# Kernel optimization log

Hardware: AMD Instinct MI355X
Metric: run time of the kernel (lower is better)

The kernel has to match this reference:

```python
import jax, jax.numpy as jnp
import numpy as np

EPS = 1e-3  # keras LayerNormalization default epsilon


def layer_norm(x, gamma, beta):
    mu = jnp.mean(x, axis=-1, keepdims=True)
    var = jnp.var(x, axis=-1, keepdims=True)
    return (x - mu) * jax.lax.rsqrt(var + EPS) * gamma + beta


def setup_inputs() -> dict:
    key = jax.random.key(0)
    ks = jax.random.split(key, 16)
    B, S, D = 8, 2048, 1024          # batch, seq, input_size
    P = 2 * D                        # up-projection dim (proj_factor=2)
    H = 1024                         # hidden = head_size(64) * num_heads(16)
    s = 0.02
    inp = {
        "x": jax.random.normal(ks[0], (B, S, D), jnp.float32),
        "ln1_g": jnp.ones((D,), jnp.float32),
        "ln1_b": jnp.zeros((D,), jnp.float32),
        "W_up": jax.random.normal(ks[1], (D, P), jnp.float32) * s,
        "b_up": jnp.zeros((P,), jnp.float32),
        "W_adj": jax.random.normal(ks[2], (P, H), jnp.float32) * s,
        "b_adj": jnp.zeros((H,), jnp.float32),
        "W_q": jax.random.normal(ks[3], (H, H), jnp.float32) * s,
        "b_q": jnp.zeros((H,), jnp.float32),
        "W_k": jax.random.normal(ks[4], (H, H), jnp.float32) * s,
        "b_k": jnp.zeros((H,), jnp.float32),
        "W_v": jax.random.normal(ks[5], (H, H), jnp.float32) * s,
        "b_v": jnp.zeros((H,), jnp.float32),
        "W_i": jax.random.normal(ks[6], (H, H), jnp.float32) * s,
        "b_i": jnp.zeros((H,), jnp.float32),
        "W_f": jax.random.normal(ks[7], (H, H), jnp.float32) * s,
        "b_f": jnp.zeros((H,), jnp.float32),
        "W_o": jax.random.normal(ks[8], (H, H), jnp.float32) * s,
        "b_o": jnp.zeros((H,), jnp.float32),
        "ln2_g": jnp.ones((H,), jnp.float32),
        "ln2_b": jnpos if False else jnp.zeros((H,), jnp.float32),
        "W_down": jax.random.normal(ks[9], (H, D), jnp.float32) * s,
        "b_down": jnp.zeros((D,), jnp.float32),
    }
    return inp


def reference(x, ln1_g, ln1_b, W_up, b_up, W_adj, b_adj,
              W_q, b_q, W_k, b_k, W_v, b_v,
              W_i, b_i, W_f, b_f, W_o, b_o,
              ln2_g, ln2_b, W_down, b_down):
    head_size = 64
    x_norm = layer_norm(x, ln1_g, ln1_b)
    x_up = x_norm @ W_up + b_up                      # [B,S,2D]
    x_adj = x_up @ W_adj + b_adj                     # [B,S,H]
    # BlockDiagonal layers: each block is a Dense over the FULL input,
    # concatenated -> equivalent to one [H,H] matmul with concatenated weights.
    q = x_adj @ W_q + b_q
    k = (x_adj @ W_k + b_k) / (head_size ** 0.5)
    v = x_adj @ W_v + b_v
    i_t = x_adj @ W_i + b_i
    f_t = x_adj @ W_f + b_f
    o = jax.nn.sigmoid(x_adj @ W_o + b_o)
    m_t = jnp.maximum(f_t, i_t)
    f = jnp.exp(f_t - m_t)                           # (i = exp(i_t - m_t) unused downstream)
    c_t = f * v * k
    h_t = o * (c_t * q) / jnp.maximum(jnp.abs(k * q), 1.0)
    out = layer_norm(h_t, ln2_g, ln2_b) * jax.nn.sigmoid(x_adj)
    out = out @ W_down + b_down
    return out + x
```

## Files before the change

kernel.cpp:

```cpp
#include <hip/hip_runtime.h>


typedef unsigned short u16;
typedef __attribute__((ext_vector_type(4))) unsigned short u16x4;
typedef __attribute__((ext_vector_type(8))) unsigned short u16x8;
typedef __attribute__((ext_vector_type(8))) __bf16 bf16x8;
typedef __attribute__((ext_vector_type(4))) float f32x4;

__device__ __forceinline__ float bf2f(u16 u) {
    union { unsigned int i; float f; } c; c.i = ((unsigned int)u) << 16; return c.f;
}
__device__ __forceinline__ u16 f2bf(float f) {
    union { float f; unsigned int i; } c; c.f = f;
    unsigned int lsb = (c.i >> 16) & 1u;
    c.i += 0x7fffu + lsb;
    return (u16)(c.i >> 16);
}
__device__ __forceinline__ float sigmoidf(float z) {
    return 1.0f / (1.0f + __expf(-z));
}

#define GLDS16(gp, lp)                                                        \
    __builtin_amdgcn_global_load_lds(                                         \
        (__attribute__((address_space(1))) void*)(void*)(gp),                 \
        (__attribute__((address_space(3))) void*)(lp), 16, 0, 0)

#define BM 128
#define BN 128
#define BK 32

template <int MODE>
__global__ __launch_bounds__(256) void gemm_bt(
    const u16* __restrict__ A, const u16* __restrict__ Bt,
    const float* __restrict__ bias, const float* __restrict__ resid,
    void* __restrict__ out, int M, int N, int K, float scale)
{
    __shared__ __align__(16) u16 As[2 * BM * BK];
    __shared__ __align__(16) u16 Bs[2 * BN * BK];

    const int tid  = threadIdx.x;
    const int lane = tid & 63;
    const int wave = tid >> 6;
    const int l15  = lane & 15;
    const int quad = lane >> 4;

    const long bm = (long)blockIdx.y * BM;
    const long bn = (long)blockIdx.x * BN;
    const int  wm = (wave >> 1) * 64;
    const int  wn = (wave & 1) * 64;

    f32x4 acc[4][4] = {};

    const int  r0 = tid >> 2;
    const int  ck = (((tid & 3) ^ ((tid >> 3) & 3)) * 8);
    const u16* ga0 = A  + (bm + r0) * (long)K + ck;
    const u16* gb0 = Bt + (bn + r0) * (long)K + ck;
    const int  ldst = wave * 512;

    auto stage = [&](int t_, int b_) {
        const long kof = (long)t_ * BK;
        u16* dA = &As[b_ * (BM * BK) + ldst];
        u16* dB = &Bs[b_ * (BN * BK) + ldst];
        GLDS16(ga0 + kof, dA);
        GLDS16(ga0 + kof + 64 * (long)K, dA + 2048);
        GLDS16(gb0 + kof, dB);
        GLDS16(gb0 + kof + 64 * (long)K, dB + 2048);
    };

    const int q8s = (quad ^ ((l15 >> 1) & 3)) * 8;
    const int nk  = K / BK;

    stage(0, 0);
    stage(1, 1);

    for (int t = 0; t < nk; ++t) {
        const int cur = t & 1;
        if (t + 1 < nk) asm volatile("s_waitcnt vmcnt(4)" ::: "memory");
        else            asm volatile("s_waitcnt vmcnt(0)" ::: "memory");
        __builtin_amdgcn_s_barrier();

        bf16x8 af[4], bfr[4];
#pragma unroll
        for (int t4 = 0; t4 < 4; ++t4) {
            af[t4]  = *(const bf16x8*)&As[cur * (BM * BK) + (wm + t4 * 16 + l15) * BK + q8s];
            bfr[t4] = *(const bf16x8*)&Bs[cur * (BN * BK) + (wn + t4 * 16 + l15) * BK + q8s];
        }
        asm volatile("s_waitcnt lgkmcnt(0)" ::: "memory");
        __builtin_amdgcn_s_barrier();
        if (t + 2 < nk) stage(t + 2, cur);

        __builtin_amdgcn_s_setprio(1);
#pragma unroll
        for (int mt = 0; mt < 4; ++mt)
#pragma unroll
            for (int nt = 0; nt < 4; ++nt)
                acc[mt][nt] = __builtin_amdgcn_mfma_f32_16x16x32_bf16(
                    af[mt], bfr[nt], acc[mt][nt], 0, 0, 0);
        __builtin_amdgcn_s_setprio(0);
    }

#pragma unroll
    for (int nt = 0; nt < 4; ++nt) {
        const long n  = bn + wn + nt * 16 + l15;
        const float bv = (MODE == 2) ? 0.0f : bias[n];
#pragma unroll
        for (int mt = 0; mt < 4; ++mt) {
            const long m0 = bm + wm + mt * 16 + quad * 4;
#pragma unroll
            for (int r = 0; r < 4; ++r) {
                const long idx = (m0 + r) * N + n;
                const float val = (acc[mt][nt][r] + bv) * scale;
                if (MODE == 1) ((float*)out)[idx] = val + resid[idx];
                else           ((u16*)out)[idx] = f2bf(val);
            }
        }
    }
}

__global__ __launch_bounds__(256) void gemm_gates(
    const u16* __restrict__ A, const u16* __restrict__ Wcat,
    const float* __restrict__ bq_, const float* __restrict__ bk_,
    const float* __restrict__ bv_, const float* __restrict__ bi_,
    const float* __restrict__ bf_, const float* __restrict__ bo_,
    u16* __restrict__ ht, int M, int N, int K)
{
    __shared__ __align__(16) u16 As[2 * 128 * 64];
    __shared__ __align__(16) u16 Bs[2 * 6 * 32 * 64];

    const int tid  = threadIdx.x;
    const int lane = tid & 63;
    const int wave = tid >> 6;
    const int l15  = lane & 15;
    const int quad = lane >> 4;

    const long bm = (long)blockIdx.y * 128;
    const long bn = (long)blockIdx.x * 32;

    f32x4 acc[6][4] = {};

    const int  rr = lane >> 3;
    const int  ck = (((lane & 7) ^ rr) * 8);

    const u16* gaj[4];
    int lAo[4];
#pragma unroll
    for (int j = 0; j < 4; ++j) {
        const int c = wave * 4 + j;
        gaj[j] = A + (bm + c * 8 + rr) * (long)K + ck;
        lAo[j] = c * 512;
    }
    const u16* gbj[6];
    int lBo[6];
#pragma unroll
    for (int j = 0; j < 6; ++j) {
        const int c = wave * 6 + j;
        const int g = c >> 2;
        const int r = (c & 3) * 8 + rr;
        gbj[j] = Wcat + ((long)g * 1024 + bn + r) * (long)K + ck;
        lBo[j] = c * 512;
    }

    auto stage = [&](int t_, int b_) {
        const long kof = (long)t_ * 64;
#pragma unroll
        for (int j = 0; j < 4; ++j)
            GLDS16(gaj[j] + kof, &As[b_ * 8192 + lAo[j]]);
#pragma unroll
        for (int j = 0; j < 6; ++j)
            GLDS16(gbj[j] + kof, &Bs[b_ * 12288 + lBo[j]]);
    };

    const int mh = (wave >> 1) * 64;
    const int nb = (wave & 1) * 16;
    const int l7 = l15 & 7;
    const int nk = K >> 6;

    stage(0, 0);
    stage(1, 1);

    for (int t = 0; t < nk; ++t) {
        const int cur = t & 1;
        if (t + 1 < nk) asm volatile("s_waitcnt vmcnt(10)" ::: "memory");
        else            asm volatile("s_waitcnt vmcnt(0)"  ::: "memory");
        __builtin_amdgcn_s_barrier();

        const int ab = cur * 8192;
        const int bb = cur * 12288;

        {
            const int so = (quad ^ l7) * 8;
            bf16x8 af[4];
#pragma unroll
            for (int t4 = 0; t4 < 4; ++t4)
                af[t4] = *(const bf16x8*)&As[ab + (mh + t4 * 16 + l15) * 64 + so];
            __builtin_amdgcn_s_setprio(1);
#pragma unroll
            for (int g = 0; g < 6; ++g) {
                const bf16x8 bfrag =
                    *(const bf16x8*)&Bs[bb + (g * 32 + nb + l15) * 64 + so];
#pragma unroll
                for (int t4 = 0; t4 < 4; ++t4)
                    acc[g][t4] = __builtin_amdgcn_mfma_f32_16x16x32_bf16(
                        af[t4], bfrag, acc[g][t4], 0, 0, 0);
            }
            __builtin_amdgcn_s_setprio(0);
        }
        bf16x8 af1[4], bf1[6];
        {
            const int so = ((4 + quad) ^ l7) * 8;
#pragma unroll
            for (int t4 = 0; t4 < 4; ++t4)
                af1[t4] = *(const bf16x8*)&As[ab + (mh + t4 * 16 + l15) * 64 + so];
#pragma unroll
            for (int g = 0; g < 6; ++g)
                bf1[g] = *(const bf16x8*)&Bs[bb + (g * 32 + nb + l15) * 64 + so];
        }
        asm volatile("s_waitcnt lgkmcnt(0)" ::: "memory");
        __builtin_amdgcn_s_barrier();
        if (t + 2 < nk) stage(t + 2, cur);

        __builtin_amdgcn_s_setprio(1);
#pragma unroll
        for (int g = 0; g < 6; ++g)
#pragma unroll
            for (int t4 = 0; t4 < 4; ++t4)
                acc[g][t4] = __builtin_amdgcn_mfma_f32_16x16x32_bf16(
                    af1[t4], bf1[g], acc[g][t4], 0, 0, 0);
        __builtin_amdgcn_s_setprio(0);
    }

    const long n = bn + nb + l15;
    const float bqn = bq_[n], bkn = bk_[n], bvn = bv_[n];
    const float bin = bi_[n], bfn = bf_[n], bon = bo_[n];
#pragma unroll
    for (int t = 0; t < 4; ++t) {
        const long m0 = bm + mh + t * 16 + quad * 4;
#pragma unroll
        for (int r = 0; r < 4; ++r) {
            const float qf = acc[0][t][r] + bqn;
            const float kf = (acc[1][t][r] + bkn) * 0.125f;
            const float vf = acc[2][t][r] + bvn;
            const float fi = acc[3][t][r] + bin;
            const float ff = acc[4][t][r] + bfn;
            const float osig = sigmoidf(acc[5][t][r] + bon);
            const float mx = fmaxf(ff, fi);
            const float fe = __expf(ff - mx);
            const float ct = fe * vf * kf;
            const float h  = osig * (ct * qf) / fmaxf(fabsf(kf * qf), 1.0f);
            ht[(m0 + r) * N + n] = f2bf(h);
        }
    }
}

__global__ __launch_bounds__(256) void ln_in_kernel(
    const float* __restrict__ x, const float* __restrict__ g,
    const float* __restrict__ b, u16* __restrict__ xn)
{
    const long row = blockIdx.x;
    const int  tid = threadIdx.x;
    const float4 v = ((const float4*)(x + row * 1024))[tid];
    float s  = v.x + v.y + v.z + v.w;
    float s2 = v.x * v.x + v.y * v.y + v.z * v.z + v.w * v.w;
#pragma unroll
    for (int off = 32; off > 0; off >>= 1) {
        s  += __shfl_down(s, off);
        s2 += __shfl_down(s2, off);
    }
    __shared__ float red[8];
    const int wave = tid >> 6;
    if ((tid & 63) == 0) { red[wave] = s; red[4 + wave] = s2; }
    __syncthreads();
    if (tid == 0) {
        const float S  = red[0] + red[1] + red[2] + red[3];
        const float S2 = red[4] + red[5] + red[6] + red[7];
        const float mu = S * (1.0f / 1024.0f);
        const float var = S2 * (1.0f / 1024.0f) - mu * mu;
        red[0] = mu; red[1] = rsqrtf(var + 1e-3f);
    }
    __syncthreads();
    const float mu = red[0], rstd = red[1];
    const int c = tid * 4;
    u16x4 o;
    o.x = f2bf((v.x - mu) * rstd * g[c + 0] + b[c + 0]);
    o.y = f2bf((v.y - mu) * rstd * g[c + 1] + b[c + 1]);
    o.z = f2bf((v.z - mu) * rstd * g[c + 2] + b[c + 2]);
    o.w = f2bf((v.w - mu) * rstd * g[c + 3] + b[c + 3]);
    *(u16x4*)(xn + row * 1024 + c) = o;
}

struct PrepArgs {
    const float *Wadj, *Wq, *Wk, *Wv, *Wi, *Wf, *Wo, *Wdn, *Wup;
    const float *bup, *badj;
    u16 *WadjT, *Wcat, *WdnT, *Wup_bf;
    float *bcomb;
};

__device__ __forceinline__ void do_transpose(
    const float* __restrict__ W, u16* __restrict__ Wt,
    int K, int N, int bx, int by, float (&t)[32][33])
{
    const int tx = threadIdx.x & 31;
    const int ty = threadIdx.x >> 5;
    const long bn = (long)bx * 32;
    const long bk = (long)by * 32;
#pragma unroll
    for (int j = 0; j < 4; ++j)
        t[ty + j * 8][tx] = W[(bk + ty + j * 8) * N + bn + tx];
    __syncthreads();
#pragma unroll
    for (int j = 0; j < 4; ++j)
        Wt[(bn + ty + j * 8) * K + bk + tx] = f2bf(t[tx][ty + j * 8]);
}

__global__ __launch_bounds__(256) void prep_kernel(PrepArgs a)
{
    __shared__ float t[32][33];
    int bid = blockIdx.x;
    if (bid < 2048) {
        do_transpose(a.Wadj, a.WadjT, 2048, 1024, bid & 31, bid >> 5, t);
        return;
    }
    bid -= 2048;
    if (bid < 6144) {
        const int g = bid >> 10, tt = bid & 1023;
        const float* Wg = g == 0 ? a.Wq : g == 1 ? a.Wk : g == 2 ? a.Wv
                        : g == 3 ? a.Wi : g == 4 ? a.Wf : a.Wo;
        do_transpose(Wg, a.Wcat + (long)g * 1024 * 1024, 1024, 1024,
                     tt & 31, tt >> 5, t);
        return;
    }
    bid -= 6144;
    if (bid < 1024) {
        do_transpose(a.Wdn, a.WdnT, 1024, 1024, bid & 31, bid >> 5, t);
        return;
    }
    bid -= 1024;
    if (bid < 2048) {
        const long i = ((long)bid * 256 + threadIdx.x) * 4;
        const float4 v = *(const float4*)(a.Wup + i);
        u16x4 o;
        o.x = f2bf(v.x); o.y = f2bf(v.y); o.z = f2bf(v.z); o.w = f2bf(v.w);
        *(u16x4*)(a.Wup_bf + i) = o;
        return;
    }
    bid -= 2048;
    {
        const int h = bid * 256 + threadIdx.x;
        float s = 0.0f;
#pragma unroll 8
        for (int p = 0; p < 2048; ++p)
            s += a.bup[p] * a.Wadj[(long)p * 1024 + h];
        a.bcomb[h] = s + a.badj[h];
    }
}

__global__ __launch_bounds__(256) void ln2_kernel(
    const u16* __restrict__ ht, const u16* __restrict__ xadj,
    const float* __restrict__ g2, const float* __restrict__ b2,
    u16* __restrict__ y)
{
    const long base = (long)blockIdx.x * 1024;
    const int  tid = threadIdx.x;
    const int  c = tid * 4;
    const u16x4 hv = *(const u16x4*)&ht[base + c];
    const u16x4 xv = *(const u16x4*)&xadj[base + c];

    float h[4];
    float s = 0.0f, s2 = 0.0f;
#pragma unroll
    for (int j = 0; j < 4; ++j) {
        h[j] = bf2f(hv[j]);
        s += h[j]; s2 += h[j] * h[j];
    }
#pragma unroll
    for (int off = 32; off > 0; off >>= 1) {
        s  += __shfl_down(s, off);
        s2 += __shfl_down(s2, off);
    }
    __shared__ float red[8];
    const int wave = tid >> 6;
    if ((tid & 63) == 0) { red[wave] = s; red[4 + wave] = s2; }
    __syncthreads();
    if (tid == 0) {
        const float S  = red[0] + red[1] + red[2] + red[3];
        const float S2 = red[4] + red[5] + red[6] + red[7];
        const float mu = S * (1.0f / 1024.0f);
        const float var = S2 * (1.0f / 1024.0f) - mu * mu;
        red[0] = mu; red[1] = rsqrtf(var + 1e-3f);
    }
    __syncthreads();
    const float mu = red[0], rstd = red[1];
    u16x4 o;
#pragma unroll
    for (int j = 0; j < 4; ++j)
        o[j] = f2bf(((h[j] - mu) * rstd * g2[c + j] + b2[c + j]) * sigmoidf(bf2f(xv[j])));
    *(u16x4*)&y[base + c] = o;
}

extern "C" void kernel_launch(void* const* d_in, const int* in_sizes, int n_in,
                              void* d_out, int out_size, void* d_ws, size_t ws_size,
                              hipStream_t stream)
{
    const float* x    = (const float*)d_in[0];
    const float* g1   = (const float*)d_in[1];
    const float* b1   = (const float*)d_in[2];
    const float* Wup  = (const float*)d_in[3];
    const float* bup  = (const float*)d_in[4];
    const float* Wadj = (const float*)d_in[5];
    const float* badj = (const float*)d_in[6];
    const float* Wq = (const float*)d_in[7];   const float* bq = (const float*)d_in[8];
    const float* Wk = (const float*)d_in[9];   const float* bk = (const float*)d_in[10];
    const float* Wv = (const float*)d_in[11];  const float* bv = (const float*)d_in[12];
    const float* Wi = (const float*)d_in[13];  const float* bi = (const float*)d_in[14];
    const float* Wf = (const float*)d_in[15];  const float* bf = (const float*)d_in[16];
    const float* Wo = (const float*)d_in[17];  const float* bo = (const float*)d_in[18];
    const float* g2 = (const float*)d_in[19];  const float* b2 = (const float*)d_in[20];
    const float* Wdn = (const float*)d_in[21]; const float* bdn = (const float*)d_in[22];

    const int M = 8 * 2048;
    const int D = 1024, P = 2048, H = 1024;

    char* ws = (char*)d_ws;
    const size_t MB = 1024 * 1024;
    u16* xn     = (u16*)(ws + 0);
    u16* htb    = (u16*)(ws + 0);
    u16* yb     = (u16*)(ws + 0);
    u16* WcombT = (u16*)(ws + 32 * MB);
    float* bcomb = (float*)(ws + 36 * MB);
    u16* xadj   = (u16*)(ws + 96 * MB);
    u16* Wup_bf = (u16*)(ws + 128 * MB);
    u16* WadjT  = (u16*)(ws + 132 * MB);
    u16* Wcat   = (u16*)(ws + 136 * MB);
    u16* WdnT   = (u16*)(ws + 148 * MB);

    ln_in_kernel<<<M, 256, 0, stream>>>(x, g1, b1, xn);

    PrepArgs pa;
    pa.Wadj = Wadj; pa.Wq = Wq; pa.Wk = Wk; pa.Wv = Wv; pa.Wi = Wi;
    pa.Wf = Wf; pa.Wo = Wo; pa.Wdn = Wdn; pa.Wup = Wup;
    pa.bup = bup; pa.badj = badj;
    pa.WadjT = WadjT; pa.Wcat = Wcat; pa.WdnT = WdnT; pa.Wup_bf = Wup_bf;
    pa.bcomb = bcomb;
    prep_kernel<<<11268, 256, 0, stream>>>(pa);

    gemm_bt<2><<<dim3(D / BN, H / BM), 256, 0, stream>>>(
        WadjT, Wup_bf, nullptr, nullptr, WcombT, H, D, P, 1.0f);

    gemm_bt<0><<<dim3(H / BN, M / BM), 256, 0, stream>>>(
        xn, WcombT, bcomb, nullptr, xadj, M, H, D, 1.0f);

    gemm_gates<<<dim3(H / 32, M / 128), 256, 0, stream>>>(
        xadj, Wcat, bq, bk, bv, bi, bf, bo, htb, M, H, H);

    ln2_kernel<<<M, 256, 0, stream>>>(htb, xadj, g2, b2, yb);

    gemm_bt<1><<<dim3(D / BN, M / BM), 256, 0, stream>>>(yb, WdnT, bdn, x, (float*)d_out, M, D, H, 1.0f);
}
```

Measured before the change: 646.5 us.

## Fuse input layernorm into prep kernel, parallelize bias combine, drop setprio

Merges the input LayerNorm kernel into the weight-prep kernel as a single launch, removing one kernel launch and the serialization between them. The combined-bias reduction now uses 32 blocks where each block splits the 2048-long dot product across 8 thread groups and reduces through shared memory, replacing 4 blocks of long serial loops. It also removes s_setprio around MFMA loops in both GEMM kernels. The bias change targets a latency-bound tail; removing setprio may change wave scheduling in either direction.

```diff
diff --git a/kernel.cpp b/kernel.cpp
--- a/kernel.cpp
+++ b/kernel.cpp
@@ -89,14 +89,12 @@
         __builtin_amdgcn_s_barrier();
         if (t + 2 < nk) stage(t + 2, cur);
 
-        __builtin_amdgcn_s_setprio(1);
 #pragma unroll
         for (int mt = 0; mt < 4; ++mt)
 #pragma unroll
             for (int nt = 0; nt < 4; ++nt)
                 acc[mt][nt] = __builtin_amdgcn_mfma_f32_16x16x32_bf16(
                     af[mt], bfr[nt], acc[mt][nt], 0, 0, 0);
-        __builtin_amdgcn_s_setprio(0);
     }
 
 #pragma unroll
@@ -193,7 +191,6 @@
 #pragma unroll
             for (int t4 = 0; t4 < 4; ++t4)
                 af[t4] = *(const bf16x8*)&As[ab + (mh + t4 * 16 + l15) * 64 + so];
-            __builtin_amdgcn_s_setprio(1);
 #pragma unroll
             for (int g = 0; g < 6; ++g) {
                 const bf16x8 bfrag =
@@ -203,7 +200,6 @@
                     acc[g][t4] = __builtin_amdgcn_mfma_f32_16x16x32_bf16(
                         af[t4], bfrag, acc[g][t4], 0, 0, 0);
             }
-            __builtin_amdgcn_s_setprio(0);
         }
         bf16x8 af1[4], bf1[6];
         {
@@ -219,14 +215,12 @@
         __builtin_amdgcn_s_barrier();
         if (t + 2 < nk) stage(t + 2, cur);
 
-        __builtin_amdgcn_s_setprio(1);
 #pragma unroll
         for (int g = 0; g < 6; ++g)
 #pragma unroll
             for (int t4 = 0; t4 < 4; ++t4)
                 acc[g][t4] = __builtin_amdgcn_mfma_f32_16x16x32_bf16(
                     af1[t4], bf1[g], acc[g][t4], 0, 0, 0);
-        __builtin_amdgcn_s_setprio(0);
     }
 
     const long n = bn + nb + l15;
@@ -252,46 +246,11 @@
     }
 }
 
-__global__ __launch_bounds__(256) void ln_in_kernel(
-    const float* __restrict__ x, const float* __restrict__ g,
-    const float* __restrict__ b, u16* __restrict__ xn)
-{
-    const long row = blockIdx.x;
-    const int  tid = threadIdx.x;
-    const float4 v = ((const float4*)(x + row * 1024))[tid];
-    float s  = v.x + v.y + v.z + v.w;
-    float s2 = v.x * v.x + v.y * v.y + v.z * v.z + v.w * v.w;
-#pragma unroll
-    for (int off = 32; off > 0; off >>= 1) {
-        s  += __shfl_down(s, off);
-        s2 += __shfl_down(s2, off);
-    }
-    __shared__ float red[8];
-    const int wave = tid >> 6;
-    if ((tid & 63) == 0) { red[wave] = s; red[4 + wave] = s2; }
-    __syncthreads();
-    if (tid == 0) {
-        const float S  = red[0] + red[1] + red[2] + red[3];
-        const float S2 = red[4] + red[5] + red[6] + red[7];
-        const float mu = S * (1.0f / 1024.0f);
-        const float var = S2 * (1.0f / 1024.0f) - mu * mu;
-        red[0] = mu; red[1] = rsqrtf(var + 1e-3f);
-    }
-    __syncthreads();
-    const float mu = red[0], rstd = red[1];
-    const int c = tid * 4;
-    u16x4 o;
-    o.x = f2bf((v.x - mu) * rstd * g[c + 0] + b[c + 0]);
-    o.y = f2bf((v.y - mu) * rstd * g[c + 1] + b[c + 1]);
-    o.z = f2bf((v.z - mu) * rstd * g[c + 2] + b[c + 2]);
-    o.w = f2bf((v.w - mu) * rstd * g[c + 3] + b[c + 3]);
-    *(u16x4*)(xn + row * 1024 + c) = o;
-}
-
-struct PrepArgs {
+struct FrontArgs {
+    const float *x, *g1, *b1;
     const float *Wadj, *Wq, *Wk, *Wv, *Wi, *Wf, *Wo, *Wdn, *Wup;
     const float *bup, *badj;
-    u16 *WadjT, *Wcat, *WdnT, *Wup_bf;
+    u16 *xn, *WadjT, *Wcat, *WdnT, *Wup_bf;
     float *bcomb;
 };
 
@@ -312,10 +271,45 @@
         Wt[(bn + ty + j * 8) * K + bk + tx] = f2bf(t[tx][ty + j * 8]);
 }
 
-__global__ __launch_bounds__(256) void prep_kernel(PrepArgs a)
+__global__ __launch_bounds__(256) void front_kernel(FrontArgs a)
 {
     __shared__ float t[32][33];
+    const int tid = threadIdx.x;
     int bid = blockIdx.x;
+
+    if (bid < 16384) {
+        const long row = bid;
+        const float4 v = ((const float4*)(a.x + row * 1024))[tid];
+        float s  = v.x + v.y + v.z + v.w;
+        float s2 = v.x * v.x + v.y * v.y + v.z * v.z + v.w * v.w;
+#pragma unroll
+        for (int off = 32; off > 0; off >>= 1) {
+            s  += __shfl_down(s, off);
+            s2 += __shfl_down(s2, off);
+        }
+        float* red = &t[0][0];
+        const int wave = tid >> 6;
+        if ((tid & 63) == 0) { red[wave] = s; red[4 + wave] = s2; }
+        __syncthreads();
+        if (tid == 0) {
+            const float S  = red[0] + red[1] + red[2] + red[3];
+            const float S2 = red[4] + red[5] + red[6] + red[7];
+            const float mu = S * (1.0f / 1024.0f);
+            const float var = S2 * (1.0f / 1024.0f) - mu * mu;
+            red[0] = mu; red[1] = rsqrtf(var + 1e-3f);
+        }
+        __syncthreads();
+        const float mu = red[0], rstd = red[1];
+        const int c = tid * 4;
+        u16x4 o;
+        o.x = f2bf((v.x - mu) * rstd * a.g1[c + 0] + a.b1[c + 0]);
+        o.y = f2bf((v.y - mu) * rstd * a.g1[c + 1] + a.b1[c + 1]);
+        o.z = f2bf((v.z - mu) * rstd * a.g1[c + 2] + a.b1[c + 2]);
+        o.w = f2bf((v.w - mu) * rstd * a.g1[c + 3] + a.b1[c + 3]);
+        *(u16x4*)(a.xn + row * 1024 + c) = o;
+        return;
+    }
+    bid -= 16384;
     if (bid < 2048) {
         do_transpose(a.Wadj, a.WadjT, 2048, 1024, bid & 31, bid >> 5, t);
         return;
@@ -336,7 +330,7 @@
     }
     bid -= 1024;
     if (bid < 2048) {
-        const long i = ((long)bid * 256 + threadIdx.x) * 4;
+        const long i = ((long)bid * 256 + tid) * 4;
         const float4 v = *(const float4*)(a.Wup + i);
         u16x4 o;
         o.x = f2bf(v.x); o.y = f2bf(v.y); o.z = f2bf(v.z); o.w = f2bf(v.w);
@@ -345,12 +339,21 @@
     }
     bid -= 2048;
     {
-        const int h = bid * 256 + threadIdx.x;
+        const int h0 = bid * 32;
+        const int hl = tid & 31;
+        const int pp = tid >> 5;
         float s = 0.0f;
-#pragma unroll 8
-        for (int p = 0; p < 2048; ++p)
-            s += a.bup[p] * a.Wadj[(long)p * 1024 + h];
-        a.bcomb[h] = s + a.badj[h];
+        for (int p = pp; p < 2048; p += 8)
+            s += a.bup[p] * a.Wadj[(long)p * 1024 + h0 + hl];
+        float* red = &t[0][0];
+        red[pp * 32 + hl] = s;
+        __syncthreads();
+        if (tid < 32) {
+            float v = 0.0f;
+#pragma unroll
+            for (int j = 0; j < 8; ++j) v += red[j * 32 + tid];
+            a.bcomb[h0 + tid] = v + a.badj[h0 + tid];
+        }
     }
 }
 
@@ -433,15 +436,14 @@
     u16* Wcat   = (u16*)(ws + 136 * MB);
     u16* WdnT   = (u16*)(ws + 148 * MB);
 
-    ln_in_kernel<<<M, 256, 0, stream>>>(x, g1, b1, xn);
-
-    PrepArgs pa;
-    pa.Wadj = Wadj; pa.Wq = Wq; pa.Wk = Wk; pa.Wv = Wv; pa.Wi = Wi;
-    pa.Wf = Wf; pa.Wo = Wo; pa.Wdn = Wdn; pa.Wup = Wup;
-    pa.bup = bup; pa.badj = badj;
-    pa.WadjT = WadjT; pa.Wcat = Wcat; pa.WdnT = WdnT; pa.Wup_bf = Wup_bf;
-    pa.bcomb = bcomb;
-    prep_kernel<<<11268, 256, 0, stream>>>(pa);
+    FrontArgs fa;
+    fa.x = x; fa.g1 = g1; fa.b1 = b1;
+    fa.Wadj = Wadj; fa.Wq = Wq; fa.Wk = Wk; fa.Wv = Wv; fa.Wi = Wi;
+    fa.Wf = Wf; fa.Wo = Wo; fa.Wdn = Wdn; fa.Wup = Wup;
+    fa.bup = bup; fa.badj = badj;
+    fa.xn = xn; fa.WadjT = WadjT; fa.Wcat = Wcat; fa.WdnT = WdnT;
+    fa.Wup_bf = Wup_bf; fa.bcomb = bcomb;
+    front_kernel<<<16384 + 2048 + 6144 + 1024 + 2048 + 32, 256, 0, stream>>>(fa);
 
     gemm_bt<2><<<dim3(D / BN, H / BM), 256, 0, stream>>>(
         WadjT, Wup_bf, nullptr, nullptr, WcombT, H, D, P, 1.0f);
```

New measurement: 615.3 us. -4.8%, faster.
